# Performance work log

Measured on AMD Instinct MI355X. Metric: run time of the kernel, lower is better.

The kernel has to match this reference:

```python
import jax, jax.numpy as jnp
import numpy as np

# Model/layout constants (match init_kwargs / input_specs)
B = 32            # decode batch (one new token per sequence)
KV_LEN = 2048     # max context length per sequence
PAGE = 16         # page size (slots per page)
PAGES = KV_LEN // PAGE   # pages per sequence (identity block table layout)
H_Q = 32          # query heads
H_KV = 8          # kv heads (GQA group = 4)
D = 128           # head dim
SCALE = 1.0 / float(np.sqrt(D))
NUM_SLOTS = B * KV_LEN   # flat cache slots (= num_pages * PAGE)


def setup_inputs() -> dict:
    key = jax.random.key(0)
    ks = jax.random.split(key, 6)
    q = jax.random.normal(ks[0], (B, H_Q, D), jnp.float32)
    k = jax.random.normal(ks[1], (B, H_KV, D), jnp.float32)
    v = jax.random.normal(ks[2], (B, H_KV, D), jnp.float32)
    # paged KV cache, flat slot-major layout: [num_slots, H_KV, D] (slot*D addressing)
    k_cache = jax.random.normal(ks[3], (NUM_SLOTS, H_KV, D), jnp.float32)
    v_cache = jax.random.normal(ks[4], (NUM_SLOTS, H_KV, D), jnp.float32)
    # identity page layout: sequence b owns pages [b*PAGES, (b+1)*PAGES)
    block_tables = (jnp.arange(B, dtype=jnp.int32)[:, None] * PAGES
                    + jnp.arange(PAGES, dtype=jnp.int32)[None, :])
    # context length INCLUDING the new token, in [1, KV_LEN]
    context_lens = jax.random.randint(ks[5], (B,), 1, KV_LEN + 1, dtype=jnp.int32)
    # slot for the new token: position ctx-1 within the sequence's page table
    pos = context_lens - 1
    page_idx = jnp.take_along_axis(block_tables, (pos // PAGE)[:, None], axis=1)[:, 0]
    slot_mapping = (page_idx * PAGE + pos % PAGE).astype(jnp.int32)
    return dict(q=q, k=k, v=v, k_cache=k_cache, v_cache=v_cache,
                slot_mapping=slot_mapping, block_tables=block_tables,
                context_lens=context_lens)


def reference(q, k, v, k_cache, v_cache, slot_mapping, block_tables, context_lens):
    # 1) store_kvcache: scatter new K/V tokens into the paged cache by flat slot
    k_cache = k_cache.at[slot_mapping].set(k)
    v_cache = v_cache.at[slot_mapping].set(v)
    # 2) paged gather: expand page table to flat slot ids [B, KV_LEN]
    slot_ids = (block_tables[:, :, None] * PAGE
                + jnp.arange(PAGE, dtype=block_tables.dtype)).reshape(B, KV_LEN)
    K = k_cache[slot_ids]  # [B, KV_LEN, H_KV, D]
    V = v_cache[slot_ids]  # [B, KV_LEN, H_KV, D]
    # 3) GQA decode attention (single query token per sequence, causal == length mask)
    G = H_Q // H_KV
    qg = q.reshape(B, H_KV, G, D)
    scores = jnp.einsum('bhgd,bkhd->bhgk', qg, K) * SCALE  # [B, H_KV, G, KV_LEN]
    valid = jnp.arange(KV_LEN)[None, None, None, :] < context_lens[:, None, None, None]
    scores = jnp.where(valid, scores, -jnp.inf)
    p = jax.nn.softmax(scores, axis=-1)
    o = jnp.einsum('bhgk,bkhd->bhgd', p, V)  # [B, H_KV, G, D]
    return o.reshape(B, H_Q, D)
```

## Files before the change

### kernel.cpp

```cpp
#include <hip/hip_runtime.h>
#include <math.h>

#define BB      32
#define H_KVN   8
#define GQ      4
#define H_QN    32
#define DD      128
#define PAGEN   16
#define PAGESN  128
#define NSPLITS 8

#define SCALE2  (0.08838834764831845f * 1.4426950408889634f)
#define NEG_INF (-__builtin_huge_valf())

__device__ __forceinline__ float row_reduce_add(float v) {
    int x;
    x = __builtin_amdgcn_update_dpp(0, __float_as_int(v), 0x128, 0xf, 0xf, true); v += __int_as_float(x);
    x = __builtin_amdgcn_update_dpp(0, __float_as_int(v), 0x124, 0xf, 0xf, true); v += __int_as_float(x);
    x = __builtin_amdgcn_update_dpp(0, __float_as_int(v), 0x122, 0xf, 0xf, true); v += __int_as_float(x);
    x = __builtin_amdgcn_update_dpp(0, __float_as_int(v), 0x121, 0xf, 0xf, true); v += __int_as_float(x);
    return v;
}

__device__ __forceinline__ float dot8(const float4& a0, const float4& a1,
                                      const float4& b0, const float4& b1) {
    return a0.x*b0.x + a0.y*b0.y + a0.z*b0.z + a0.w*b0.w
         + a1.x*b1.x + a1.y*b1.y + a1.z*b1.z + a1.w*b1.w;
}

__global__ __launch_bounds__(256)
void paged_decode_partial(const float* __restrict__ q,
                          const float* __restrict__ knew,
                          const float* __restrict__ vnew,
                          const float* __restrict__ kcache,
                          const float* __restrict__ vcache,
                          const int*   __restrict__ btab,
                          const int*   __restrict__ ctx_lens,
                          float*       __restrict__ ws_o,
                          float*       __restrict__ ws_ml)
{
    const int bid = blockIdx.x;
    const int s   = bid % NSPLITS;
    const int bh  = bid / NSPLITS;
    const int h   = bh % H_KVN;
    const int b   = bh / H_KVN;
    const int tid  = threadIdx.x;
    const int w    = tid >> 6;
    const int lane = tid & 63;
    const int g16  = lane >> 4;
    const int l16  = lane & 15;

    const int ctx   = ctx_lens[b];
    const int chunk = (((ctx + NSPLITS - 1) / NSPLITS) + 15) & ~15;
    const int start = s * chunk;
    const int end   = min(start + chunk, ctx);
    const int cend  = min(end, ctx - 1);
    const int span  = cend - start;
    const int nfull = (span > 0) ? (span & ~31) : 0;

    float4 qa[GQ], qb[GQ];
    {
        const float* qp = q + ((size_t)b * H_QN + (size_t)h * GQ) * DD + l16 * 8;
        #pragma unroll
        for (int g = 0; g < GQ; ++g) {
            qa[g] = *(const float4*)(qp + g * DD);
            qb[g] = *(const float4*)(qp + g * DD + 4);
        }
    }

    float m[GQ], l[GQ], o[GQ][8];
    #pragma unroll
    for (int g = 0; g < GQ; ++g) {
        m[g] = NEG_INF; l[g] = 0.f;
        #pragma unroll
        for (int j = 0; j < 8; ++j) o[g][j] = 0.f;
    }

    const int* btb = btab + b * PAGESN;

    if (w == 0 && g16 == 0 && start <= ctx - 1 && ctx - 1 < end) {
        const size_t off = ((size_t)b * H_KVN + h) * DD + l16 * 8;
        const float4 ka = *(const float4*)(knew + off);
        const float4 kb = *(const float4*)(knew + off + 4);
        const float4 va = *(const float4*)(vnew + off);
        const float4 vb = *(const float4*)(vnew + off + 4);
        const float ve[8] = { va.x, va.y, va.z, va.w, vb.x, vb.y, vb.z, vb.w };
        #pragma unroll
        for (int g = 0; g < GQ; ++g) {
            float d0 = row_reduce_add(dot8(qa[g], qb[g], ka, kb));
            m[g] = d0 * SCALE2;
            l[g] = 1.f;
            #pragma unroll
            for (int j = 0; j < 8; ++j) o[g][j] = ve[j];
        }
    }

    for (int p0 = start + w * 8; p0 < start + nfull; p0 += 32) {
        const int pA = p0 + g16;
        const int pB = pA + 4;
        const int slotA = btb[pA >> 4] * PAGEN + (pA & (PAGEN - 1));
        const int slotB = btb[pB >> 4] * PAGEN + (pB & (PAGEN - 1));
        const size_t offA = ((size_t)slotA * H_KVN + h) * DD + l16 * 8;
        const size_t offB = ((size_t)slotB * H_KVN + h) * DD + l16 * 8;
        const float4 kA0 = *(const float4*)(kcache + offA);
        const float4 kA1 = *(const float4*)(kcache + offA + 4);
        const float4 vA0 = *(const float4*)(vcache + offA);
        const float4 vA1 = *(const float4*)(vcache + offA + 4);
        const float4 kB0 = *(const float4*)(kcache + offB);
        const float4 kB1 = *(const float4*)(kcache + offB + 4);
        const float4 vB0 = *(const float4*)(vcache + offB);
        const float4 vB1 = *(const float4*)(vcache + offB + 4);

        float dA[GQ], dB[GQ];
        #pragma unroll
        for (int g = 0; g < GQ; ++g) {
            dA[g] = dot8(qa[g], qb[g], kA0, kA1);
            dB[g] = dot8(qa[g], qb[g], kB0, kB1);
        }
        #pragma unroll
        for (int g = 0; g < GQ; ++g) {
            dA[g] = row_reduce_add(dA[g]);
            dB[g] = row_reduce_add(dB[g]);
        }
        const float vAe[8] = { vA0.x, vA0.y, vA0.z, vA0.w, vA1.x, vA1.y, vA1.z, vA1.w };
        const float vBe[8] = { vB0.x, vB0.y, vB0.z, vB0.w, vB1.x, vB1.y, vB1.z, vB1.w };
        #pragma unroll
        for (int g = 0; g < GQ; ++g) {
            const float scA  = dA[g] * SCALE2;
            const float scB  = dB[g] * SCALE2;
            const float nm   = fmaxf(m[g], fmaxf(scA, scB));
            const float corr = exp2f(m[g] - nm);
            const float pa   = exp2f(scA - nm);
            const float pb   = exp2f(scB - nm);
            l[g] = l[g] * corr + pa + pb;
            m[g] = nm;
            #pragma unroll
            for (int j = 0; j < 8; ++j)
                o[g][j] = o[g][j] * corr + pa * vAe[j] + pb * vBe[j];
        }
    }

    for (int p = start + nfull + w * 4 + g16; p < cend; p += 16) {
        const int slot = btb[p >> 4] * PAGEN + (p & (PAGEN - 1));
        const size_t off = ((size_t)slot * H_KVN + h) * DD + l16 * 8;
        const float4 k0 = *(const float4*)(kcache + off);
        const float4 k1 = *(const float4*)(kcache + off + 4);
        const float4 v0 = *(const float4*)(vcache + off);
        const float4 v1 = *(const float4*)(vcache + off + 4);
        float d[GQ];
        #pragma unroll
        for (int g = 0; g < GQ; ++g) d[g] = dot8(qa[g], qb[g], k0, k1);
        #pragma unroll
        for (int g = 0; g < GQ; ++g) d[g] = row_reduce_add(d[g]);
        const float ve[8] = { v0.x, v0.y, v0.z, v0.w, v1.x, v1.y, v1.z, v1.w };
        #pragma unroll
        for (int g = 0; g < GQ; ++g) {
            const float sc   = d[g] * SCALE2;
            const float nm   = fmaxf(m[g], sc);
            const float corr = exp2f(m[g] - nm);
            const float pw   = exp2f(sc - nm);
            l[g] = l[g] * corr + pw;
            m[g] = nm;
            #pragma unroll
            for (int j = 0; j < 8; ++j)
                o[g][j] = o[g][j] * corr + pw * ve[j];
        }
    }

    #pragma unroll
    for (int msk = 16; msk <= 32; msk <<= 1) {
        #pragma unroll
        for (int g = 0; g < GQ; ++g) {
            const float mo = __shfl_xor(m[g], msk);
            const float lo = __shfl_xor(l[g], msk);
            const float M  = fmaxf(m[g], mo);
            const float c1 = (m[g] == NEG_INF) ? 0.f : exp2f(m[g] - M);
            const float c2 = (mo   == NEG_INF) ? 0.f : exp2f(mo   - M);
            l[g] = l[g] * c1 + lo * c2;
            #pragma unroll
            for (int j = 0; j < 8; ++j) {
                const float oo = __shfl_xor(o[g][j], msk);
                o[g][j] = o[g][j] * c1 + oo * c2;
            }
            m[g] = M;
        }
    }

    __shared__ float o_lds[4][GQ][DD];
    __shared__ float m_lds[4][GQ];
    __shared__ float l_lds[4][GQ];
    if (g16 == 0) {
        #pragma unroll
        for (int g = 0; g < GQ; ++g)
            #pragma unroll
            for (int j = 0; j < 8; ++j)
                o_lds[w][g][l16 * 8 + j] = o[g][j];
    }
    if (lane == 0) {
        #pragma unroll
        for (int g = 0; g < GQ; ++g) { m_lds[w][g] = m[g]; l_lds[w][g] = l[g]; }
    }
    __syncthreads();

    const size_t idx = (size_t)bh * NSPLITS + s;
    float* op  = ws_o  + idx * (GQ * DD);
    float* mlp = ws_ml + idx * (GQ * 2);

    for (int e = tid; e < GQ * DD; e += 256) {
        const int g = e >> 7;
        const int d = e & (DD - 1);
        const float M = fmaxf(fmaxf(m_lds[0][g], m_lds[1][g]),
                              fmaxf(m_lds[2][g], m_lds[3][g]));
        float acc = 0.f;
        #pragma unroll
        for (int ww = 0; ww < 4; ++ww) {
            const float mw  = m_lds[ww][g];
            const float wgt = (mw == NEG_INF) ? 0.f : exp2f(mw - M);
            acc += o_lds[ww][g][d] * wgt;
        }
        op[e] = acc;
    }
    if (tid < GQ) {
        const int g = tid;
        const float M = fmaxf(fmaxf(m_lds[0][g], m_lds[1][g]),
                              fmaxf(m_lds[2][g], m_lds[3][g]));
        float L = 0.f;
        #pragma unroll
        for (int ww = 0; ww < 4; ++ww) {
            const float mw  = m_lds[ww][g];
            const float wgt = (mw == NEG_INF) ? 0.f : exp2f(mw - M);
            L += l_lds[ww][g] * wgt;
        }
        mlp[g * 2]     = M;
        mlp[g * 2 + 1] = L;
    }
}

__global__ __launch_bounds__(256)
void paged_decode_reduce(const float* __restrict__ ws_o,
                         const float* __restrict__ ws_ml,
                         float*       __restrict__ out)
{
    const int bh  = blockIdx.x;
    const int tid = threadIdx.x;
    __shared__ float ML[GQ][2];

    const float* mlp = ws_ml + (size_t)bh * NSPLITS * (GQ * 2);
    if (tid < GQ) {
        const int g = tid;
        float M = NEG_INF;
        for (int s = 0; s < NSPLITS; ++s)
            M = fmaxf(M, mlp[s * GQ * 2 + g * 2]);
        float L = 0.f;
        for (int s = 0; s < NSPLITS; ++s) {
            const float mw  = mlp[s * GQ * 2 + g * 2];
            const float wgt = (mw == NEG_INF) ? 0.f : exp2f(mw - M);
            L += mlp[s * GQ * 2 + g * 2 + 1] * wgt;
        }
        ML[g][0] = M;
        ML[g][1] = L;
    }
    __syncthreads();

    const float* op = ws_o + (size_t)bh * NSPLITS * (GQ * DD);
    const int b = bh / H_KVN, h = bh % H_KVN;
    float* outp = out + ((size_t)b * H_QN + (size_t)h * GQ) * DD;

    for (int e = tid; e < GQ * DD; e += 256) {
        const int g = e >> 7;
        const float M = ML[g][0], L = ML[g][1];
        float acc = 0.f;
        for (int s = 0; s < NSPLITS; ++s) {
            const float mw  = mlp[s * GQ * 2 + g * 2];
            const float wgt = (mw == NEG_INF) ? 0.f : exp2f(mw - M);
            acc += op[s * GQ * DD + e] * wgt;
        }
        outp[e] = acc / L;
    }
}

extern "C" void kernel_launch(void* const* d_in, const int* in_sizes, int n_in,
                              void* d_out, int out_size, void* d_ws, size_t ws_size,
                              hipStream_t stream) {
    const float* q  = (const float*)d_in[0];
    const float* k  = (const float*)d_in[1];
    const float* v  = (const float*)d_in[2];
    const float* kc = (const float*)d_in[3];
    const float* vc = (const float*)d_in[4];
    const int* bt   = (const int*)d_in[6];
    const int* ctx  = (const int*)d_in[7];
    float* out = (float*)d_out;

    float* ws_o  = (float*)d_ws;
    float* ws_ml = ws_o + (size_t)BB * H_KVN * NSPLITS * (GQ * DD);

    paged_decode_partial<<<BB * H_KVN * NSPLITS, 256, 0, stream>>>(
        q, k, v, kc, vc, bt, ctx, ws_o, ws_ml);
    paged_decode_reduce<<<BB * H_KVN, 256, 0, stream>>>(ws_o, ws_ml, out);
}
```

Before: 60.01 us.

## Double KV splits, fold softmax scale into Q, vectorize split-combine

Raises the number of KV-length splits per (batch, kv-head) from 8 to 16, giving more blocks for a memory-bound decode with variable context lengths. Pre-multiplies Q by the softmax scale once so the per-token score multiply disappears from the inner loops. The combine kernel now has each of 128 threads handle a float4 across all splits instead of a scalar strided loop. More splits mean more partial-result workspace traffic and more combine work, and shorter chunks per block.

```diff
diff --git a/kernel.cpp b/kernel.cpp
--- a/kernel.cpp
+++ b/kernel.cpp
@@ -8,7 +8,7 @@
 #define DD      128
 #define PAGEN   16
 #define PAGESN  128
-#define NSPLITS 8
+#define NSPLITS 16
 
 #define SCALE2  (0.08838834764831845f * 1.4426950408889634f)
 #define NEG_INF (-__builtin_huge_valf())
@@ -63,8 +63,11 @@
         const float* qp = q + ((size_t)b * H_QN + (size_t)h * GQ) * DD + l16 * 8;
         #pragma unroll
         for (int g = 0; g < GQ; ++g) {
-            qa[g] = *(const float4*)(qp + g * DD);
-            qb[g] = *(const float4*)(qp + g * DD + 4);
+            float4 a = *(const float4*)(qp + g * DD);
+            float4 c = *(const float4*)(qp + g * DD + 4);
+            a.x *= SCALE2; a.y *= SCALE2; a.z *= SCALE2; a.w *= SCALE2;
+            c.x *= SCALE2; c.y *= SCALE2; c.z *= SCALE2; c.w *= SCALE2;
+            qa[g] = a; qb[g] = c;
         }
     }
 
@@ -87,8 +90,7 @@
         const float ve[8] = { va.x, va.y, va.z, va.w, vb.x, vb.y, vb.z, vb.w };
         #pragma unroll
         for (int g = 0; g < GQ; ++g) {
-            float d0 = row_reduce_add(dot8(qa[g], qb[g], ka, kb));
-            m[g] = d0 * SCALE2;
+            m[g] = row_reduce_add(dot8(qa[g], qb[g], ka, kb));
             l[g] = 1.f;
             #pragma unroll
             for (int j = 0; j < 8; ++j) o[g][j] = ve[j];
@@ -126,8 +128,8 @@
         const float vBe[8] = { vB0.x, vB0.y, vB0.z, vB0.w, vB1.x, vB1.y, vB1.z, vB1.w };
         #pragma unroll
         for (int g = 0; g < GQ; ++g) {
-            const float scA  = dA[g] * SCALE2;
-            const float scB  = dB[g] * SCALE2;
+            const float scA  = dA[g];
+            const float scB  = dB[g];
             const float nm   = fmaxf(m[g], fmaxf(scA, scB));
             const float corr = exp2f(m[g] - nm);
             const float pa   = exp2f(scA - nm);
@@ -155,7 +157,7 @@
         const float ve[8] = { v0.x, v0.y, v0.z, v0.w, v1.x, v1.y, v1.z, v1.w };
         #pragma unroll
         for (int g = 0; g < GQ; ++g) {
-            const float sc   = d[g] * SCALE2;
+            const float sc   = d[g];
             const float nm   = fmaxf(m[g], sc);
             const float corr = exp2f(m[g] - nm);
             const float pw   = exp2f(sc - nm);
@@ -262,21 +264,26 @@
     }
     __syncthreads();
 
-    const float* op = ws_o + (size_t)bh * NSPLITS * (GQ * DD);
+    if (tid >= (GQ * DD) / 4) return;
+    const int e4 = tid;
+    const int g  = (e4 * 4) >> 7;
+    const float M = ML[g][0], L = ML[g][1];
+
+    const float4* op4 = (const float4*)(ws_o + (size_t)bh * NSPLITS * (GQ * DD));
+    float4 acc = make_float4(0.f, 0.f, 0.f, 0.f);
+    for (int s = 0; s < NSPLITS; ++s) {
+        const float mw  = mlp[s * GQ * 2 + g * 2];
+        const float wgt = (mw == NEG_INF) ? 0.f : exp2f(mw - M);
+        const float4 v  = op4[s * (GQ * DD / 4) + e4];
+        acc.x += v.x * wgt; acc.y += v.y * wgt;
+        acc.z += v.z * wgt; acc.w += v.w * wgt;
+    }
+    const float inv = 1.f / L;
+    acc.x *= inv; acc.y *= inv; acc.z *= inv; acc.w *= inv;
+
     const int b = bh / H_KVN, h = bh % H_KVN;
-    float* outp = out + ((size_t)b * H_QN + (size_t)h * GQ) * DD;
-
-    for (int e = tid; e < GQ * DD; e += 256) {
-        const int g = e >> 7;
-        const float M = ML[g][0], L = ML[g][1];
-        float acc = 0.f;
-        for (int s = 0; s < NSPLITS; ++s) {
-            const float mw  = mlp[s * GQ * 2 + g * 2];
-            const float wgt = (mw == NEG_INF) ? 0.f : exp2f(mw - M);
-            acc += op[s * GQ * DD + e] * wgt;
-        }
-        outp[e] = acc / L;
-    }
+    float4* outp = (float4*)(out + ((size_t)b * H_QN + (size_t)h * GQ) * DD);
+    outp[e4] = acc;
 }
 
 extern "C" void kernel_launch(void* const* d_in, const int* in_sizes, int n_in,
```

Result: faster. 55.86 us (-6.9%).
